# Kernel tuning notes

Measured on AMD Instinct MI355X. Metric: run time of the kernel, lower is better.

Reference implementation:

```python
import jax, jax.numpy as jnp
import numpy as np

H = 16  # heads
K_POLY = 3  # K from init


def setup_inputs() -> dict:
    key = jax.random.key(0)
    ks = jax.random.split(key, 6)
    B, N, D = 4, 1024, 1024
    s = 1.0 / np.sqrt(D)
    return {
        "x": jax.random.normal(ks[0], (B, N, D), jnp.float32),
        "Wq": jax.random.normal(ks[1], (D, D), jnp.float32) * s,
        "bq": jnp.zeros((D,), jnp.float32),
        "Wk": jax.random.normal(ks[2], (D, D), jnp.float32) * s,
        "bk": jnp.zeros((D,), jnp.float32),
        "Wv": jax.random.normal(ks[3], (D, D), jnp.float32) * s,
        "bv": jnp.zeros((D,), jnp.float32),
        "Wo": jax.random.normal(ks[4], (D, D), jnp.float32) * s,
        "bo": jnp.zeros((D,), jnp.float32),
        "w0": jnp.zeros((H,), jnp.float32),
        "w1": jnp.ones((H,), jnp.float32),
        "wK": jnp.zeros((H,), jnp.float32),
    }


def reference(x, Wq, bq, Wk, bk, Wv, bv, Wo, bo, w0, w1, wK):
    B, N, D = x.shape
    d = D // H
    # projections -> [B, H, N, d]
    def proj(W, b):
        return (x @ W + b).reshape(B, N, H, d).transpose(0, 2, 1, 3)
    q = proj(Wq, bq)
    k = proj(Wk, bk)
    v = proj(Wv, bv)
    att = jax.nn.softmax(jnp.einsum('bhnd,bhmd->bhnm', q, k) / jnp.sqrt(jnp.float32(d)), axis=-1)
    att2 = jnp.einsum('bhnm,bhmk->bhnk', att, att)  # att @ att
    attK = att + (K_POLY - 1) * (att2 - att)
    eye = jnp.eye(N, dtype=x.dtype)  # [N, N]
    gf = (w0[None, :, None, None] * eye[None, None]
          + w1[None, :, None, None] * att
          + wK[None, :, None, None] * attK)
    out = jnp.einsum('bhnm,bhmd->bhnd', gf, v)  # [B, H, N, d]
    out = out.transpose(0, 2, 1, 3).reshape(B, N, D)
    return out @ Wo + bo
```

## Files before the change

### kernel.cpp

```cpp
#include <hip/hip_runtime.h>

typedef unsigned short u16;
typedef unsigned int u32;
typedef __attribute__((ext_vector_type(8))) short short8;
typedef __attribute__((ext_vector_type(4))) float f32x4;

__device__ __forceinline__ u16 f2bf(float f) {
  union { float f; u32 u; } c; c.f = f;
  u32 u = c.u;
  u += 0x7fffu + ((u >> 16) & 1u);
  return (u16)(u >> 16);
}
__device__ __forceinline__ float bf2f(u16 h) {
  union { u32 u; float f; } c; c.u = ((u32)h) << 16;
  return c.f;
}

#define GLDS16(g, l)                                                          \
  __builtin_amdgcn_global_load_lds(                                           \
      (const __attribute__((address_space(1))) u32*)(g),                      \
      (__attribute__((address_space(3))) u32*)(l), 16, 0, 0)

__global__ __launch_bounds__(256) void k_cast_x(const float* __restrict__ x,
                                                u16* __restrict__ xb) {
  int i = blockIdx.x * 256 + threadIdx.x;
  float4 v = ((const float4*)x)[i];
  short4 s;
  s.x = (short)f2bf(v.x); s.y = (short)f2bf(v.y);
  s.z = (short)f2bf(v.z); s.w = (short)f2bf(v.w);
  *(short4*)(xb + (size_t)i * 4) = s;
}

__global__ __launch_bounds__(256) void k_trans_w(
    const float* __restrict__ W0, const float* __restrict__ W1,
    const float* __restrict__ W2, const float* __restrict__ W3,
    u16* __restrict__ T0, u16* __restrict__ T1, u16* __restrict__ T2,
    u16* __restrict__ T3) {
  const float* W = blockIdx.z == 0 ? W0 : blockIdx.z == 1 ? W1 : blockIdx.z == 2 ? W2 : W3;
  u16* T = blockIdx.z == 0 ? T0 : blockIdx.z == 1 ? T1 : blockIdx.z == 2 ? T2 : T3;
  __shared__ float tile[32][33];
  int r0 = blockIdx.y * 32, c0 = blockIdx.x * 32;
  int tid = threadIdx.x;
  for (int i = tid; i < 1024; i += 256) {
    int r = i >> 5, c = i & 31;
    tile[r][c] = W[(size_t)(r0 + r) * 1024 + c0 + c];
  }
  __syncthreads();
  for (int i = tid; i < 1024; i += 256) {
    int r = i >> 5, c = i & 31;
    T[(size_t)(c0 + r) * 1024 + r0 + c] = f2bf(tile[c][r]);
  }
}

__device__ __forceinline__ void core128x128_p3(const u16* __restrict__ A,
                                               const u16* __restrict__ Bt, int K,
                                               f32x4 (&acc)[4][4], u16* As,
                                               u16* Bs) {
  const int tid = threadIdx.x;
  const int lane = tid & 63;
  const int wm = tid >> 7, wn = (tid >> 6) & 1;
  const int fr = lane & 15, fg = lane >> 4;
  const int sr = tid >> 2, sc = (tid & 3) * 8;
#pragma unroll
  for (int i = 0; i < 4; ++i)
#pragma unroll
    for (int j = 0; j < 4; ++j) acc[i][j] = f32x4{0.f, 0.f, 0.f, 0.f};

  auto stage = [&](int t, int slot) {
    u16* as = As + slot * 4096;
    u16* bs = Bs + slot * 4096;
    const int k0 = t * 32 + sc;
    GLDS16(A + (size_t)sr * K + k0, as + tid * 8);
    GLDS16(A + (size_t)(sr + 64) * K + k0, as + (256 + tid) * 8);
    GLDS16(Bt + (size_t)sr * K + k0, bs + tid * 8);
    GLDS16(Bt + (size_t)(sr + 64) * K + k0, bs + (256 + tid) * 8);
  };
  auto compute = [&](int slot) {
    const u16* as = As + slot * 4096;
    const u16* bs = Bs + slot * 4096;
    short8 af[4], bfv[4];
#pragma unroll
    for (int i = 0; i < 4; ++i)
      af[i] = *(const short8*)(as + (wm * 64 + i * 16 + fr) * 32 + fg * 8);
#pragma unroll
    for (int j = 0; j < 4; ++j)
      bfv[j] = *(const short8*)(bs + (wn * 64 + j * 16 + fr) * 32 + fg * 8);
#pragma unroll
    for (int i = 0; i < 4; ++i)
#pragma unroll
      for (int j = 0; j < 4; ++j)
        acc[i][j] = __builtin_amdgcn_mfma_f32_16x16x32_bf16(af[i], bfv[j],
                                                            acc[i][j], 0, 0, 0);
  };

  const int NS = K / 32;
  stage(0, 0);
  stage(1, 1);
  int cs = 0, ss = 2;
  for (int t = 0; t + 2 < NS; ++t) {
    asm volatile("s_waitcnt vmcnt(4)" ::: "memory");
    __builtin_amdgcn_s_barrier();
    asm volatile("" ::: "memory");
    stage(t + 2, ss);
    compute(cs);
    cs = cs == 2 ? 0 : cs + 1;
    ss = ss == 2 ? 0 : ss + 1;
  }
  asm volatile("s_waitcnt vmcnt(4)" ::: "memory");
  __builtin_amdgcn_s_barrier();
  asm volatile("" ::: "memory");
  compute(cs);
  cs = cs == 2 ? 0 : cs + 1;
  asm volatile("s_waitcnt vmcnt(0)" ::: "memory");
  __builtin_amdgcn_s_barrier();
  asm volatile("" ::: "memory");
  compute(cs);
}

__device__ __forceinline__ void core128x64_p3(const u16* __restrict__ A,
                                              const u16* __restrict__ Bt, int K,
                                              f32x4 (&acc)[2][4], u16* As,
                                              u16* Bs) {
  const int tid = threadIdx.x;
  const int lane = tid & 63;
  const int w = tid >> 6;
  const int fr = lane & 15, fg = lane >> 4;
  const int sr = tid >> 2, sc = (tid & 3) * 8;
#pragma unroll
  for (int i = 0; i < 2; ++i)
#pragma unroll
    for (int j = 0; j < 4; ++j) acc[i][j] = f32x4{0.f, 0.f, 0.f, 0.f};

  auto stage = [&](int t, int slot) {
    u16* as = As + slot * 4096;
    u16* bs = Bs + slot * 2048;
    const int k0 = t * 32 + sc;
    GLDS16(A + (size_t)sr * K + k0, as + tid * 8);
    GLDS16(A + (size_t)(sr + 64) * K + k0, as + (256 + tid) * 8);
    GLDS16(Bt + (size_t)sr * K + k0, bs + tid * 8);
  };
  auto compute = [&](int slot) {
    const u16* as = As + slot * 4096;
    const u16* bs = Bs + slot * 2048;
    short8 af[2], bfv[4];
#pragma unroll
    for (int i = 0; i < 2; ++i)
      af[i] = *(const short8*)(as + (w * 32 + i * 16 + fr) * 32 + fg * 8);
#pragma unroll
    for (int j = 0; j < 4; ++j)
      bfv[j] = *(const short8*)(bs + (j * 16 + fr) * 32 + fg * 8);
#pragma unroll
    for (int i = 0; i < 2; ++i)
#pragma unroll
      for (int j = 0; j < 4; ++j)
        acc[i][j] = __builtin_amdgcn_mfma_f32_16x16x32_bf16(af[i], bfv[j],
                                                            acc[i][j], 0, 0, 0);
  };

  const int NS = K / 32;
  stage(0, 0);
  stage(1, 1);
  int cs = 0, ss = 2;
  for (int t = 0; t + 2 < NS; ++t) {
    asm volatile("s_waitcnt vmcnt(3)" ::: "memory");
    __builtin_amdgcn_s_barrier();
    asm volatile("" ::: "memory");
    stage(t + 2, ss);
    compute(cs);
    cs = cs == 2 ? 0 : cs + 1;
    ss = ss == 2 ? 0 : ss + 1;
  }
  asm volatile("s_waitcnt vmcnt(3)" ::: "memory");
  __builtin_amdgcn_s_barrier();
  asm volatile("" ::: "memory");
  compute(cs);
  cs = cs == 2 ? 0 : cs + 1;
  asm volatile("s_waitcnt vmcnt(0)" ::: "memory");
  __builtin_amdgcn_s_barrier();
  asm volatile("" ::: "memory");
  compute(cs);
}

__global__ __launch_bounds__(256) void k_proj(
    const u16* __restrict__ xb, const u16* __restrict__ WqT,
    const u16* __restrict__ WkT, const u16* __restrict__ WvT,
    const float* __restrict__ bq, const float* __restrict__ bk,
    const float* __restrict__ bv, u16* __restrict__ qh, u16* __restrict__ kh,
    u16* __restrict__ vh, u16* __restrict__ vT) {
  __shared__ __align__(16) u16 As[3 * 128 * 32];
  __shared__ __align__(16) u16 Bs[3 * 128 * 32];
  const int which = blockIdx.z;
  const u16* Bt = which == 0 ? WqT : which == 1 ? WkT : WvT;
  const float* bias = which == 0 ? bq : which == 1 ? bk : bv;
  const int m0 = blockIdx.x * 128, n0 = blockIdx.y * 128;
  f32x4 acc[4][4];
  core128x128_p3(xb + (size_t)m0 * 1024, Bt + (size_t)n0 * 1024, 1024, acc, As, Bs);
  const int tid = threadIdx.x, lane = tid & 63;
  const int wm = tid >> 7, wn = (tid >> 6) & 1, fr = lane & 15, fg = lane >> 4;
#pragma unroll
  for (int i = 0; i < 4; ++i)
#pragma unroll
    for (int j = 0; j < 4; ++j) {
      int n = n0 + wn * 64 + j * 16 + fr;
      float bb = bias[n];
      int h = n >> 6, dc = n & 63;
#pragma unroll
      for (int r = 0; r < 4; ++r) {
        int m = m0 + wm * 64 + i * 16 + fg * 4 + r;
        int b = m >> 10, nr = m & 1023;
        int z = b * 16 + h;
        float val = acc[i][j][r] + bb;
        u16 bv16 = f2bf(val);
        if (which == 0) {
          qh[((size_t)z * 1024 + nr) * 64 + dc] = bv16;
        } else if (which == 1) {
          kh[((size_t)z * 1024 + nr) * 64 + dc] = bv16;
        } else {
          vh[((size_t)z * 1024 + nr) * 64 + dc] = bv16;
          vT[((size_t)z * 64 + dc) * 1024 + nr] = bv16;
        }
      }
    }
}

__global__ __launch_bounds__(256) void k_pass1(
    const u16* __restrict__ qh, const u16* __restrict__ kh,
    const u16* __restrict__ vT, u16* __restrict__ P1T,
    u16* __restrict__ P1h, float2* __restrict__ ml) {
  __shared__ __align__(16) u16 Ks[64 * 64];
  __shared__ __align__(16) u16 Vs[64 * 64];
  __shared__ __align__(16) u16 Ps[4][32 * 64];
  const int z = blockIdx.y;
  const int m0 = blockIdx.x * 128;
  const int tid = threadIdx.x, lane = tid & 63, w = tid >> 6;
  const int fr = lane & 15, fg = lane >> 4;
  const int row0 = m0 + w * 32;
  const u16* qbase = qh + (size_t)z * 65536;
  const u16* kbase = kh + (size_t)z * 65536;
  const u16* vbase = vT + (size_t)z * 65536;
  u16* myP = &Ps[w][0];

  short8 qf[2][2];
#pragma unroll
  for (int rt = 0; rt < 2; ++rt)
#pragma unroll
    for (int kc = 0; kc < 2; ++kc)
      qf[rt][kc] = *(const short8*)(qbase + (size_t)(row0 + rt * 16 + fr) * 64 +
                                    (kc * 4 + fg) * 8);

  f32x4 o[2][4];
  float mr[2][4], lr[2][4];
#pragma unroll
  for (int rt = 0; rt < 2; ++rt)
#pragma unroll
    for (int ct = 0; ct < 4; ++ct) o[rt][ct] = f32x4{0.f, 0.f, 0.f, 0.f};
#pragma unroll
  for (int rt = 0; rt < 2; ++rt)
#pragma unroll
    for (int r = 0; r < 4; ++r) { mr[rt][r] = -3.0e38f; lr[rt][r] = 0.f; }

  for (int t = 0; t < 16; ++t) {
    const int kv0 = t * 64;
#pragma unroll
    for (int it = 0; it < 2; ++it) {
      int idx = it * 256 + tid;
      int row = idx >> 3, cc = idx & 7;
      GLDS16(kbase + (size_t)(kv0 + row) * 64 + ((cc ^ (row & 7)) * 8),
             Ks + idx * 8);
      GLDS16(vbase + (size_t)row * 1024 + kv0 + ((cc ^ (row & 7)) * 8),
             Vs + idx * 8);
    }
    __syncthreads();
    f32x4 s[2][4];
#pragma unroll
    for (int ct = 0; ct < 4; ++ct) {
      int krow = ct * 16 + fr;
      short8 k0 = *(const short8*)(Ks + krow * 64 + ((fg ^ (krow & 7)) * 8));
      short8 k1 = *(const short8*)(Ks + krow * 64 + (((4 + fg) ^ (krow & 7)) * 8));
#pragma unroll
      for (int rt = 0; rt < 2; ++rt) {
        s[rt][ct] = __builtin_amdgcn_mfma_f32_16x16x32_bf16(
            qf[rt][0], k0, f32x4{0.f, 0.f, 0.f, 0.f}, 0, 0, 0);
        s[rt][ct] = __builtin_amdgcn_mfma_f32_16x16x32_bf16(
            qf[rt][1], k1, s[rt][ct], 0, 0, 0);
      }
    }
    float nm[2][4], rs[2][4], al[2][4];
#pragma unroll
    for (int rt = 0; rt < 2; ++rt)
#pragma unroll
      for (int r = 0; r < 4; ++r)
        nm[rt][r] = fmaxf(fmaxf(s[rt][0][r], s[rt][1][r]),
                          fmaxf(s[rt][2][r], s[rt][3][r]));
#pragma unroll
    for (int off = 1; off < 16; off <<= 1)
#pragma unroll
      for (int rt = 0; rt < 2; ++rt)
#pragma unroll
        for (int r = 0; r < 4; ++r)
          nm[rt][r] = fmaxf(nm[rt][r], __shfl_xor(nm[rt][r], off, 64));
#pragma unroll
    for (int rt = 0; rt < 2; ++rt)
#pragma unroll
      for (int r = 0; r < 4; ++r) {
        float m_ = fmaxf(nm[rt][r], mr[rt][r]);
        al[rt][r] = __expf((mr[rt][r] - m_) * 0.125f);
        nm[rt][r] = m_;
        rs[rt][r] = 0.f;
      }
#pragma unroll
    for (int ct = 0; ct < 4; ++ct)
#pragma unroll
      for (int rt = 0; rt < 2; ++rt)
#pragma unroll
        for (int r = 0; r < 4; ++r) {
          float e = __expf((s[rt][ct][r] - nm[rt][r]) * 0.125f);
          s[rt][ct][r] = e;
          rs[rt][r] += e;
        }
#pragma unroll
    for (int off = 1; off < 16; off <<= 1)
#pragma unroll
      for (int rt = 0; rt < 2; ++rt)
#pragma unroll
        for (int r = 0; r < 4; ++r)
          rs[rt][r] += __shfl_xor(rs[rt][r], off, 64);
#pragma unroll
    for (int rt = 0; rt < 2; ++rt)
#pragma unroll
      for (int r = 0; r < 4; ++r) {
        lr[rt][r] = lr[rt][r] * al[rt][r] + rs[rt][r];
        mr[rt][r] = nm[rt][r];
      }
#pragma unroll
    for (int rt = 0; rt < 2; ++rt)
#pragma unroll
      for (int ct = 0; ct < 4; ++ct)
#pragma unroll
        for (int r = 0; r < 4; ++r) o[rt][ct][r] *= al[rt][r];
#pragma unroll
    for (int rt = 0; rt < 2; ++rt)
#pragma unroll
      for (int ct = 0; ct < 4; ++ct)
#pragma unroll
        for (int r = 0; r < 4; ++r) {
          int prow = rt * 16 + fg * 4 + r;
          int pcol = ct * 16 + fr;
          int cc = pcol >> 3;
          myP[prow * 64 + ((cc ^ (prow & 7)) * 8) + (pcol & 7)] =
              f2bf(s[rt][ct][r]);
        }
    asm volatile("s_waitcnt lgkmcnt(0)" ::: "memory");
#pragma unroll
    for (int rt = 0; rt < 2; ++rt) {
      int prow = rt * 16 + fr;
      short8 p0 = *(const short8*)(myP + prow * 64 + ((fg ^ (prow & 7)) * 8));
      short8 p1 = *(const short8*)(myP + prow * 64 + (((4 + fg) ^ (prow & 7)) * 8));
#pragma unroll
      for (int ct = 0; ct < 4; ++ct) {
        int vrow = ct * 16 + fr;
        short8 v0 = *(const short8*)(Vs + vrow * 64 + ((fg ^ (vrow & 7)) * 8));
        short8 v1 = *(const short8*)(Vs + vrow * 64 + (((4 + fg) ^ (vrow & 7)) * 8));
        o[rt][ct] = __builtin_amdgcn_mfma_f32_16x16x32_bf16(p0, v0, o[rt][ct], 0, 0, 0);
        o[rt][ct] = __builtin_amdgcn_mfma_f32_16x16x32_bf16(p1, v1, o[rt][ct], 0, 0, 0);
      }
    }
    __syncthreads();
  }
  float linv[2][4];
#pragma unroll
  for (int rt = 0; rt < 2; ++rt)
#pragma unroll
    for (int r = 0; r < 4; ++r) linv[rt][r] = 1.f / lr[rt][r];
#pragma unroll
  for (int rt = 0; rt < 2; ++rt)
#pragma unroll
    for (int ct = 0; ct < 4; ++ct) {
      union { u16 u[4]; short4 s4; } pk;
#pragma unroll
      for (int r = 0; r < 4; ++r) {
        u16 b_ = f2bf(o[rt][ct][r] * linv[rt][r]);
        pk.u[r] = b_;
        myP[(rt * 16 + fg * 4 + r) * 64 + ct * 16 + fr] = b_;
      }
      *(short4*)(P1T + ((size_t)z * 64 + ct * 16 + fr) * 1024 + row0 +
                 rt * 16 + fg * 4) = pk.s4;
    }
  asm volatile("s_waitcnt lgkmcnt(0)" ::: "memory");
  {
    int r_ = lane >> 1, hb = lane & 1;
#pragma unroll
    for (int c = 0; c < 4; ++c) {
      int ch = hb * 4 + c;
      int4 vv = *(const int4*)(myP + r_ * 64 + ch * 8);
      *(int4*)(P1h + ((size_t)z * 1024 + row0 + r_) * 64 + ch * 8) = vv;
    }
  }
  if (fr == 0) {
#pragma unroll
    for (int rt = 0; rt < 2; ++rt)
#pragma unroll
      for (int r = 0; r < 4; ++r)
        ml[(size_t)z * 1024 + row0 + rt * 16 + fg * 4 + r] =
            make_float2(mr[rt][r], linv[rt][r]);
  }
}

__global__ __launch_bounds__(256) void k_pass2(
    const u16* __restrict__ qh, const u16* __restrict__ kh,
    const u16* __restrict__ P1T, const u16* __restrict__ vh,
    const u16* __restrict__ P1h, const float2* __restrict__ ml,
    const float* __restrict__ w0, const float* __restrict__ w1,
    const float* __restrict__ wK, u16* __restrict__ OH) {
  __shared__ __align__(16) u16 Ks[64 * 64];
  __shared__ __align__(16) u16 Ts[64 * 64];
  __shared__ __align__(16) u16 Ps[4][32 * 64];
  const int z = blockIdx.y;
  const int m0 = blockIdx.x * 128;
  const int tid = threadIdx.x, lane = tid & 63, w = tid >> 6;
  const int fr = lane & 15, fg = lane >> 4;
  const int row0 = m0 + w * 32;
  const int h = z & 15, b = z >> 4;
  const float c0 = w0[h], c1 = w1[h] - wK[h], c2 = 2.f * wK[h];
  const u16* qbase = qh + (size_t)z * 65536;
  const u16* kbase = kh + (size_t)z * 65536;
  const u16* tbase = P1T + (size_t)z * 65536;
  u16* myP = &Ps[w][0];

  short8 qf[2][2];
#pragma unroll
  for (int rt = 0; rt < 2; ++rt)
#pragma unroll
    for (int kc = 0; kc < 2; ++kc)
      qf[rt][kc] = *(const short8*)(qbase + (size_t)(row0 + rt * 16 + fr) * 64 +
                                    (kc * 4 + fg) * 8);
  float mrow[2][4], lrow[2][4];
#pragma unroll
  for (int rt = 0; rt < 2; ++rt)
#pragma unroll
    for (int r = 0; r < 4; ++r) {
      float2 t_ = ml[(size_t)z * 1024 + row0 + rt * 16 + fg * 4 + r];
      mrow[rt][r] = t_.x;
      lrow[rt][r] = t_.y;
    }
  f32x4 o[2][4];
#pragma unroll
  for (int rt = 0; rt < 2; ++rt)
#pragma unroll
    for (int ct = 0; ct < 4; ++ct) o[rt][ct] = f32x4{0.f, 0.f, 0.f, 0.f};

  for (int t = 0; t < 16; ++t) {
    const int kv0 = t * 64;
#pragma unroll
    for (int it = 0; it < 2; ++it) {
      int idx = it * 256 + tid;
      int row = idx >> 3, cc = idx & 7;
      GLDS16(kbase + (size_t)(kv0 + row) * 64 + ((cc ^ (row & 7)) * 8),
             Ks + idx * 8);
      GLDS16(tbase + (size_t)row * 1024 + kv0 + ((cc ^ (row & 7)) * 8),
             Ts + idx * 8);
    }
    __syncthreads();
    f32x4 s[2][4];
#pragma unroll
    for (int ct = 0; ct < 4; ++ct) {
      int krow = ct * 16 + fr;
      short8 k0 = *(const short8*)(Ks + krow * 64 + ((fg ^ (krow & 7)) * 8));
      short8 k1 = *(const short8*)(Ks + krow * 64 + (((4 + fg) ^ (krow & 7)) * 8));
#pragma unroll
      for (int rt = 0; rt < 2; ++rt) {
        s[rt][ct] = __builtin_amdgcn_mfma_f32_16x16x32_bf16(
            qf[rt][0], k0, f32x4{0.f, 0.f, 0.f, 0.f}, 0, 0, 0);
        s[rt][ct] = __builtin_amdgcn_mfma_f32_16x16x32_bf16(
            qf[rt][1], k1, s[rt][ct], 0, 0, 0);
      }
    }
#pragma unroll
    for (int rt = 0; rt < 2; ++rt)
#pragma unroll
      for (int ct = 0; ct < 4; ++ct)
#pragma unroll
        for (int r = 0; r < 4; ++r) {
          int prow = rt * 16 + fg * 4 + r;
          int pcol = ct * 16 + fr;
          int cc = pcol >> 3;
          float p = __expf((s[rt][ct][r] - mrow[rt][r]) * 0.125f) * lrow[rt][r];
          myP[prow * 64 + ((cc ^ (prow & 7)) * 8) + (pcol & 7)] = f2bf(p);
        }
    asm volatile("s_waitcnt lgkmcnt(0)" ::: "memory");
#pragma unroll
    for (int rt = 0; rt < 2; ++rt) {
      int prow = rt * 16 + fr;
      short8 p0 = *(const short8*)(myP + prow * 64 + ((fg ^ (prow & 7)) * 8));
      short8 p1 = *(const short8*)(myP + prow * 64 + (((4 + fg) ^ (prow & 7)) * 8));
#pragma unroll
      for (int ct = 0; ct < 4; ++ct) {
        int vrow = ct * 16 + fr;
        short8 v0 = *(const short8*)(Ts + vrow * 64 + ((fg ^ (vrow & 7)) * 8));
        short8 v1 = *(const short8*)(Ts + vrow * 64 + (((4 + fg) ^ (vrow & 7)) * 8));
        o[rt][ct] = __builtin_amdgcn_mfma_f32_16x16x32_bf16(p0, v0, o[rt][ct], 0, 0, 0);
        o[rt][ct] = __builtin_amdgcn_mfma_f32_16x16x32_bf16(p1, v1, o[rt][ct], 0, 0, 0);
      }
    }
    __syncthreads();
  }
#pragma unroll
  for (int rt = 0; rt < 2; ++rt)
#pragma unroll
    for (int ct = 0; ct < 4; ++ct)
#pragma unroll
      for (int r = 0; r < 4; ++r)
        myP[(rt * 16 + fg * 4 + r) * 64 + ct * 16 + fr] = f2bf(o[rt][ct][r]);
  asm volatile("s_waitcnt lgkmcnt(0)" ::: "memory");
  {
    int r_ = lane >> 1, hb = lane & 1;
    const u16* vp = vh + ((size_t)z * 1024 + row0 + r_) * 64;
    const u16* pp = P1h + ((size_t)z * 1024 + row0 + r_) * 64;
    u16* op = OH + ((size_t)b * 1024 + row0 + r_) * 1024 + h * 64;
#pragma unroll
    for (int c = 0; c < 4; ++c) {
      int ch = hb * 4 + c;
      short8 pv = *(const short8*)(myP + r_ * 64 + ch * 8);
      short8 vv = *(const short8*)(vp + ch * 8);
      short8 p1 = *(const short8*)(pp + ch * 8);
      short8 res;
#pragma unroll
      for (int e = 0; e < 8; ++e) {
        float f = c0 * bf2f((u16)vv[e]) + c1 * bf2f((u16)p1[e]) +
                  c2 * bf2f((u16)pv[e]);
        res[e] = (short)f2bf(f);
      }
      *(short8*)(op + ch * 8) = res;
    }
  }
}

__global__ __launch_bounds__(256) void k_final(const u16* __restrict__ OH,
                                               const u16* __restrict__ WoT,
                                               const float* __restrict__ bo,
                                               float* __restrict__ out) {
  __shared__ __align__(16) u16 As[3 * 128 * 32];
  __shared__ __align__(16) u16 Bs[3 * 64 * 32];
  const int m0 = blockIdx.x * 128, n0 = blockIdx.y * 64;
  f32x4 acc[2][4];
  core128x64_p3(OH + (size_t)m0 * 1024, WoT + (size_t)n0 * 1024, 1024, acc, As, Bs);
  const int tid = threadIdx.x, lane = tid & 63, w = tid >> 6;
  const int fr = lane & 15, fg = lane >> 4;
#pragma unroll
  for (int i = 0; i < 2; ++i)
#pragma unroll
    for (int j = 0; j < 4; ++j) {
      int n = n0 + j * 16 + fr;
      float bb = bo[n];
#pragma unroll
      for (int r = 0; r < 4; ++r) {
        int m = m0 + w * 32 + i * 16 + fg * 4 + r;
        out[(size_t)m * 1024 + n] = acc[i][j][r] + bb;
      }
    }
}

extern "C" void kernel_launch(void* const* d_in, const int* in_sizes, int n_in,
                              void* d_out, int out_size, void* d_ws,
                              size_t ws_size, hipStream_t stream) {
  const float* x = (const float*)d_in[0];
  const float* Wq = (const float*)d_in[1];
  const float* bq = (const float*)d_in[2];
  const float* Wk = (const float*)d_in[3];
  const float* bk = (const float*)d_in[4];
  const float* Wv = (const float*)d_in[5];
  const float* bv = (const float*)d_in[6];
  const float* Wo = (const float*)d_in[7];
  const float* bo = (const float*)d_in[8];
  const float* w0 = (const float*)d_in[9];
  const float* w1 = (const float*)d_in[10];
  const float* wK = (const float*)d_in[11];
  float* out = (float*)d_out;

  char* ws = (char*)d_ws;
  const size_t MB = 1ull << 20;
  u16* xb  = (u16*)(ws);
  u16* WqT = (u16*)(ws + 8 * MB);
  u16* WkT = (u16*)(ws + 10 * MB);
  u16* WvT = (u16*)(ws + 12 * MB);
  u16* WoT = (u16*)(ws + 14 * MB);
  u16* qh  = (u16*)(ws + 16 * MB);
  u16* kh  = (u16*)(ws + 24 * MB);
  u16* vh  = (u16*)(ws + 32 * MB);
  u16* vT  = (u16*)(ws + 40 * MB);
  u16* P1T = (u16*)(ws + 48 * MB);
  u16* P1h = (u16*)(ws + 56 * MB);
  u16* OH  = (u16*)(ws + 64 * MB);
  float2* ml = (float2*)(ws + 72 * MB);

  hipLaunchKernelGGL(k_cast_x, dim3(4096), dim3(256), 0, stream, x, xb);
  hipLaunchKernelGGL(k_trans_w, dim3(32, 32, 4), dim3(256), 0, stream, Wq, Wk,
                     Wv, Wo, WqT, WkT, WvT, WoT);
  hipLaunchKernelGGL(k_proj, dim3(32, 8, 3), dim3(256), 0, stream, xb, WqT, WkT,
                     WvT, bq, bk, bv, qh, kh, vh, vT);
  hipLaunchKernelGGL(k_pass1, dim3(8, 64), dim3(256), 0, stream, qh, kh, vT,
                     P1T, P1h, ml);
  hipLaunchKernelGGL(k_pass2, dim3(8, 64), dim3(256), 0, stream, qh, kh, P1T,
                     vh, P1h, ml, w0, w1, wK, OH);
  hipLaunchKernelGGL(k_final, dim3(32, 16), dim3(256), 0, stream, OH, WoT, bo,
                     out);
}
```

Before: 182.5 us.

## Drop online-softmax max tracking and halve attention row tiles per block

```diff
diff --git a/kernel.cpp b/kernel.cpp
--- a/kernel.cpp
+++ b/kernel.cpp
@@ -20,6 +20,8 @@
   __builtin_amdgcn_global_load_lds(                                           \
       (const __attribute__((address_space(1))) u32*)(g),                      \
       (__attribute__((address_space(3))) u32*)(l), 16, 0, 0)
+
+#define EXP_SCALE 0.18033688011112042f
 
 __global__ __launch_bounds__(256) void k_cast_x(const float* __restrict__ x,
                                                 u16* __restrict__ xb) {
@@ -226,38 +228,31 @@
 __global__ __launch_bounds__(256) void k_pass1(
     const u16* __restrict__ qh, const u16* __restrict__ kh,
     const u16* __restrict__ vT, u16* __restrict__ P1T,
-    u16* __restrict__ P1h, float2* __restrict__ ml) {
+    u16* __restrict__ P1h, float* __restrict__ mlinv) {
   __shared__ __align__(16) u16 Ks[64 * 64];
   __shared__ __align__(16) u16 Vs[64 * 64];
-  __shared__ __align__(16) u16 Ps[4][32 * 64];
+  __shared__ __align__(16) u16 Ps[4][16 * 64];
   const int z = blockIdx.y;
-  const int m0 = blockIdx.x * 128;
+  const int m0 = blockIdx.x * 64;
   const int tid = threadIdx.x, lane = tid & 63, w = tid >> 6;
   const int fr = lane & 15, fg = lane >> 4;
-  const int row0 = m0 + w * 32;
+  const int row0 = m0 + w * 16;
   const u16* qbase = qh + (size_t)z * 65536;
   const u16* kbase = kh + (size_t)z * 65536;
   const u16* vbase = vT + (size_t)z * 65536;
   u16* myP = &Ps[w][0];
 
-  short8 qf[2][2];
-#pragma unroll
-  for (int rt = 0; rt < 2; ++rt)
-#pragma unroll
-    for (int kc = 0; kc < 2; ++kc)
-      qf[rt][kc] = *(const short8*)(qbase + (size_t)(row0 + rt * 16 + fr) * 64 +
-                                    (kc * 4 + fg) * 8);
-
-  f32x4 o[2][4];
-  float mr[2][4], lr[2][4];
-#pragma unroll
-  for (int rt = 0; rt < 2; ++rt)
-#pragma unroll
-    for (int ct = 0; ct < 4; ++ct) o[rt][ct] = f32x4{0.f, 0.f, 0.f, 0.f};
-#pragma unroll
-  for (int rt = 0; rt < 2; ++rt)
-#pragma unroll
-    for (int r = 0; r < 4; ++r) { mr[rt][r] = -3.0e38f; lr[rt][r] = 0.f; }
+  short8 qf[2];
+#pragma unroll
+  for (int kc = 0; kc < 2; ++kc)
+    qf[kc] = *(const short8*)(qbase + (size_t)(row0 + fr) * 64 + (kc * 4 + fg) * 8);
+
+  f32x4 o[4];
+  float rs[4];
+#pragma unroll
+  for (int ct = 0; ct < 4; ++ct) o[ct] = f32x4{0.f, 0.f, 0.f, 0.f};
+#pragma unroll
+  for (int r = 0; r < 4; ++r) rs[r] = 0.f;
 
   for (int t = 0; t < 16; ++t) {
     const int kv0 = t * 64;
@@ -271,155 +266,87 @@
              Vs + idx * 8);
     }
     __syncthreads();
-    f32x4 s[2][4];
 #pragma unroll
     for (int ct = 0; ct < 4; ++ct) {
       int krow = ct * 16 + fr;
       short8 k0 = *(const short8*)(Ks + krow * 64 + ((fg ^ (krow & 7)) * 8));
       short8 k1 = *(const short8*)(Ks + krow * 64 + (((4 + fg) ^ (krow & 7)) * 8));
-#pragma unroll
-      for (int rt = 0; rt < 2; ++rt) {
-        s[rt][ct] = __builtin_amdgcn_mfma_f32_16x16x32_bf16(
-            qf[rt][0], k0, f32x4{0.f, 0.f, 0.f, 0.f}, 0, 0, 0);
-        s[rt][ct] = __builtin_amdgcn_mfma_f32_16x16x32_bf16(
-            qf[rt][1], k1, s[rt][ct], 0, 0, 0);
+      f32x4 s = __builtin_amdgcn_mfma_f32_16x16x32_bf16(
+          qf[0], k0, f32x4{0.f, 0.f, 0.f, 0.f}, 0, 0, 0);
+      s = __builtin_amdgcn_mfma_f32_16x16x32_bf16(qf[1], k1, s, 0, 0, 0);
+      int pcol = ct * 16 + fr;
+      int cc = pcol >> 3;
+#pragma unroll
+      for (int r = 0; r < 4; ++r) {
+        float e = __builtin_exp2f(s[r] * EXP_SCALE);
+        rs[r] += e;
+        int prow = fg * 4 + r;
+        myP[prow * 64 + ((cc ^ (prow & 7)) * 8) + (pcol & 7)] = f2bf(e);
       }
     }
-    float nm[2][4], rs[2][4], al[2][4];
-#pragma unroll
-    for (int rt = 0; rt < 2; ++rt)
-#pragma unroll
-      for (int r = 0; r < 4; ++r)
-        nm[rt][r] = fmaxf(fmaxf(s[rt][0][r], s[rt][1][r]),
-                          fmaxf(s[rt][2][r], s[rt][3][r]));
-#pragma unroll
-    for (int off = 1; off < 16; off <<= 1)
-#pragma unroll
-      for (int rt = 0; rt < 2; ++rt)
-#pragma unroll
-        for (int r = 0; r < 4; ++r)
-          nm[rt][r] = fmaxf(nm[rt][r], __shfl_xor(nm[rt][r], off, 64));
-#pragma unroll
-    for (int rt = 0; rt < 2; ++rt)
-#pragma unroll
-      for (int r = 0; r < 4; ++r) {
-        float m_ = fmaxf(nm[rt][r], mr[rt][r]);
-        al[rt][r] = __expf((mr[rt][r] - m_) * 0.125f);
-        nm[rt][r] = m_;
-        rs[rt][r] = 0.f;
-      }
-#pragma unroll
-    for (int ct = 0; ct < 4; ++ct)
-#pragma unroll
-      for (int rt = 0; rt < 2; ++rt)
-#pragma unroll
-        for (int r = 0; r < 4; ++r) {
-          float e = __expf((s[rt][ct][r] - nm[rt][r]) * 0.125f);
-          s[rt][ct][r] = e;
-          rs[rt][r] += e;
-        }
-#pragma unroll
-    for (int off = 1; off < 16; off <<= 1)
-#pragma unroll
-      for (int rt = 0; rt < 2; ++rt)
-#pragma unroll
-        for (int r = 0; r < 4; ++r)
-          rs[rt][r] += __shfl_xor(rs[rt][r], off, 64);
-#pragma unroll
-    for (int rt = 0; rt < 2; ++rt)
-#pragma unroll
-      for (int r = 0; r < 4; ++r) {
-        lr[rt][r] = lr[rt][r] * al[rt][r] + rs[rt][r];
-        mr[rt][r] = nm[rt][r];
-      }
-#pragma unroll
-    for (int rt = 0; rt < 2; ++rt)
-#pragma unroll
-      for (int ct = 0; ct < 4; ++ct)
-#pragma unroll
-        for (int r = 0; r < 4; ++r) o[rt][ct][r] *= al[rt][r];
-#pragma unroll
-    for (int rt = 0; rt < 2; ++rt)
-#pragma unroll
-      for (int ct = 0; ct < 4; ++ct)
-#pragma unroll
-        for (int r = 0; r < 4; ++r) {
-          int prow = rt * 16 + fg * 4 + r;
-          int pcol = ct * 16 + fr;
-          int cc = pcol >> 3;
-          myP[prow * 64 + ((cc ^ (prow & 7)) * 8) + (pcol & 7)] =
-              f2bf(s[rt][ct][r]);
-        }
     asm volatile("s_waitcnt lgkmcnt(0)" ::: "memory");
-#pragma unroll
-    for (int rt = 0; rt < 2; ++rt) {
-      int prow = rt * 16 + fr;
-      short8 p0 = *(const short8*)(myP + prow * 64 + ((fg ^ (prow & 7)) * 8));
-      short8 p1 = *(const short8*)(myP + prow * 64 + (((4 + fg) ^ (prow & 7)) * 8));
-#pragma unroll
-      for (int ct = 0; ct < 4; ++ct) {
-        int vrow = ct * 16 + fr;
-        short8 v0 = *(const short8*)(Vs + vrow * 64 + ((fg ^ (vrow & 7)) * 8));
-        short8 v1 = *(const short8*)(Vs + vrow * 64 + (((4 + fg) ^ (vrow & 7)) * 8));
-        o[rt][ct] = __builtin_amdgcn_mfma_f32_16x16x32_bf16(p0, v0, o[rt][ct], 0, 0, 0);
-        o[rt][ct] = __builtin_amdgcn_mfma_f32_16x16x32_bf16(p1, v1, o[rt][ct], 0, 0, 0);
-      }
+    short8 p0 = *(const short8*)(myP + fr * 64 + ((fg ^ (fr & 7)) * 8));
+    short8 p1 = *(const short8*)(myP + fr * 64 + (((4 + fg) ^ (fr & 7)) * 8));
+#pragma unroll
+    for (int ct = 0; ct < 4; ++ct) {
+      int vrow = ct * 16 + fr;
+      short8 v0 = *(const short8*)(Vs + vrow * 64 + ((fg ^ (vrow & 7)) * 8));
+      short8 v1 = *(const short8*)(Vs + vrow * 64 + (((4 + fg) ^ (vrow & 7)) * 8));
+      o[ct] = __builtin_amdgcn_mfma_f32_16x16x32_bf16(p0, v0, o[ct], 0, 0, 0);
+      o[ct] = __builtin_amdgcn_mfma_f32_16x16x32_bf16(p1, v1, o[ct], 0, 0, 0);
     }
     __syncthreads();
   }
-  float linv[2][4];
-#pragma unroll
-  for (int rt = 0; rt < 2; ++rt)
-#pragma unroll
-    for (int r = 0; r < 4; ++r) linv[rt][r] = 1.f / lr[rt][r];
-#pragma unroll
-  for (int rt = 0; rt < 2; ++rt)
-#pragma unroll
-    for (int ct = 0; ct < 4; ++ct) {
-      union { u16 u[4]; short4 s4; } pk;
-#pragma unroll
-      for (int r = 0; r < 4; ++r) {
-        u16 b_ = f2bf(o[rt][ct][r] * linv[rt][r]);
-        pk.u[r] = b_;
-        myP[(rt * 16 + fg * 4 + r) * 64 + ct * 16 + fr] = b_;
-      }
-      *(short4*)(P1T + ((size_t)z * 64 + ct * 16 + fr) * 1024 + row0 +
-                 rt * 16 + fg * 4) = pk.s4;
-    }
+#pragma unroll
+  for (int off = 1; off < 16; off <<= 1)
+#pragma unroll
+    for (int r = 0; r < 4; ++r) rs[r] += __shfl_xor(rs[r], off, 64);
+  float linv[4];
+#pragma unroll
+  for (int r = 0; r < 4; ++r) linv[r] = 1.f / rs[r];
+#pragma unroll
+  for (int ct = 0; ct < 4; ++ct) {
+    union { u16 u[4]; short4 s4; } pk;
+#pragma unroll
+    for (int r = 0; r < 4; ++r) {
+      u16 b_ = f2bf(o[ct][r] * linv[r]);
+      pk.u[r] = b_;
+      myP[(fg * 4 + r) * 64 + ct * 16 + fr] = b_;
+    }
+    *(short4*)(P1T + ((size_t)z * 64 + ct * 16 + fr) * 1024 + row0 + fg * 4) =
+        pk.s4;
+  }
   asm volatile("s_waitcnt lgkmcnt(0)" ::: "memory");
   {
-    int r_ = lane >> 1, hb = lane & 1;
-#pragma unroll
-    for (int c = 0; c < 4; ++c) {
-      int ch = hb * 4 + c;
+    int r_ = lane >> 2;
+#pragma unroll
+    for (int c = 0; c < 2; ++c) {
+      int ch = (lane & 3) * 2 + c;
       int4 vv = *(const int4*)(myP + r_ * 64 + ch * 8);
       *(int4*)(P1h + ((size_t)z * 1024 + row0 + r_) * 64 + ch * 8) = vv;
     }
   }
   if (fr == 0) {
 #pragma unroll
-    for (int rt = 0; rt < 2; ++rt)
-#pragma unroll
-      for (int r = 0; r < 4; ++r)
-        ml[(size_t)z * 1024 + row0 + rt * 16 + fg * 4 + r] =
-            make_float2(mr[rt][r], linv[rt][r]);
+    for (int r = 0; r < 4; ++r)
+      mlinv[(size_t)z * 1024 + row0 + fg * 4 + r] = linv[r];
   }
 }
 
 __global__ __launch_bounds__(256) void k_pass2(
     const u16* __restrict__ qh, const u16* __restrict__ kh,
     const u16* __restrict__ P1T, const u16* __restrict__ vh,
-    const u16* __restrict__ P1h, const float2* __restrict__ ml,
+    const u16* __restrict__ P1h, const float* __restrict__ mlinv,
     const float* __restrict__ w0, const float* __restrict__ w1,
     const float* __restrict__ wK, u16* __restrict__ OH) {
   __shared__ __align__(16) u16 Ks[64 * 64];
   __shared__ __align__(16) u16 Ts[64 * 64];
-  __shared__ __align__(16) u16 Ps[4][32 * 64];
+  __shared__ __align__(16) u16 Ps[4][16 * 64];
   const int z = blockIdx.y;
-  const int m0 = blockIdx.x * 128;
+  const int m0 = blockIdx.x * 64;
   const int tid = threadIdx.x, lane = tid & 63, w = tid >> 6;
   const int fr = lane & 15, fg = lane >> 4;
-  const int row0 = m0 + w * 32;
+  const int row0 = m0 + w * 16;
   const int h = z & 15, b = z >> 4;
   const float c0 = w0[h], c1 = w1[h] - wK[h], c2 = 2.f * wK[h];
   const u16* qbase = qh + (size_t)z * 65536;
@@ -427,27 +354,17 @@
   const u16* tbase = P1T + (size_t)z * 65536;
   u16* myP = &Ps[w][0];
 
-  short8 qf[2][2];
-#pragma unroll
-  for (int rt = 0; rt < 2; ++rt)
-#pragma unroll
-    for (int kc = 0; kc < 2; ++kc)
-      qf[rt][kc] = *(const short8*)(qbase + (size_t)(row0 + rt * 16 + fr) * 64 +
-                                    (kc * 4 + fg) * 8);
-  float mrow[2][4], lrow[2][4];
-#pragma unroll
-  for (int rt = 0; rt < 2; ++rt)
-#pragma unroll
-    for (int r = 0; r < 4; ++r) {
-      float2 t_ = ml[(size_t)z * 1024 + row0 + rt * 16 + fg * 4 + r];
-      mrow[rt][r] = t_.x;
-      lrow[rt][r] = t_.y;
-    }
-  f32x4 o[2][4];
-#pragma unroll
-  for (int rt = 0; rt < 2; ++rt)
-#pragma unroll
-    for (int ct = 0; ct < 4; ++ct) o[rt][ct] = f32x4{0.f, 0.f, 0.f, 0.f};
+  short8 qf[2];
+#pragma unroll
+  for (int kc = 0; kc < 2; ++kc)
+    qf[kc] = *(const short8*)(qbase + (size_t)(row0 + fr) * 64 + (kc * 4 + fg) * 8);
+  float lrow[4];
+#pragma unroll
+  for (int r = 0; r < 4; ++r)
+    lrow[r] = mlinv[(size_t)z * 1024 + row0 + fg * 4 + r];
+  f32x4 o[4];
+#pragma unroll
+  for (int ct = 0; ct < 4; ++ct) o[ct] = f32x4{0.f, 0.f, 0.f, 0.f};
 
   for (int t = 0; t < 16; ++t) {
     const int kv0 = t * 64;
@@ -461,65 +378,50 @@
              Ts + idx * 8);
     }
     __syncthreads();
-    f32x4 s[2][4];
 #pragma unroll
     for (int ct = 0; ct < 4; ++ct) {
       int krow = ct * 16 + fr;
       short8 k0 = *(const short8*)(Ks + krow * 64 + ((fg ^ (krow & 7)) * 8));
       short8 k1 = *(const short8*)(Ks + krow * 64 + (((4 + fg) ^ (krow & 7)) * 8));
-#pragma unroll
-      for (int rt = 0; rt < 2; ++rt) {
-        s[rt][ct] = __builtin_amdgcn_mfma_f32_16x16x32_bf16(
-            qf[rt][0], k0, f32x4{0.f, 0.f, 0.f, 0.f}, 0, 0, 0);
-        s[rt][ct] = __builtin_amdgcn_mfma_f32_16x16x32_bf16(
-            qf[rt][1], k1, s[rt][ct], 0, 0, 0);
+      f32x4 s = __builtin_amdgcn_mfma_f32_16x16x32_bf16(
+          qf[0], k0, f32x4{0.f, 0.f, 0.f, 0.f}, 0, 0, 0);
+      s = __builtin_amdgcn_mfma_f32_16x16x32_bf16(qf[1], k1, s, 0, 0, 0);
+      int pcol = ct * 16 + fr;
+      int cc = pcol >> 3;
+#pragma unroll
+      for (int r = 0; r < 4; ++r) {
+        float p = __builtin_exp2f(s[r] * EXP_SCALE) * lrow[r];
+        int prow = fg * 4 + r;
+        myP[prow * 64 + ((cc ^ (prow & 7)) * 8) + (pcol & 7)] = f2bf(p);
       }
     }
-#pragma unroll
-    for (int rt = 0; rt < 2; ++rt)
-#pragma unroll
-      for (int ct = 0; ct < 4; ++ct)
-#pragma unroll
-        for (int r = 0; r < 4; ++r) {
-          int prow = rt * 16 + fg * 4 + r;
-          int pcol = ct * 16 + fr;
-          int cc = pcol >> 3;
-          float p = __expf((s[rt][ct][r] - mrow[rt][r]) * 0.125f) * lrow[rt][r];
-          myP[prow * 64 + ((cc ^ (prow & 7)) * 8) + (pcol & 7)] = f2bf(p);
-        }
     asm volatile("s_waitcnt lgkmcnt(0)" ::: "memory");
-#pragma unroll
-    for (int rt = 0; rt < 2; ++rt) {
-      int prow = rt * 16 + fr;
-      short8 p0 = *(const short8*)(myP + prow * 64 + ((fg ^ (prow & 7)) * 8));
-      short8 p1 = *(const short8*)(myP + prow * 64 + (((4 + fg) ^ (prow & 7)) * 8));
-#pragma unroll
-      for (int ct = 0; ct < 4; ++ct) {
-        int vrow = ct * 16 + fr;
-        short8 v0 = *(const short8*)(Ts + vrow * 64 + ((fg ^ (vrow & 7)) * 8));
-        short8 v1 = *(const short8*)(Ts + vrow * 64 + (((4 + fg) ^ (vrow & 7)) * 8));
-        o[rt][ct] = __builtin_amdgcn_mfma_f32_16x16x32_bf16(p0, v0, o[rt][ct], 0, 0, 0);
-        o[rt][ct] = __builtin_amdgcn_mfma_f32_16x16x32_bf16(p1, v1, o[rt][ct], 0, 0, 0);
-      }
+    short8 p0 = *(const short8*)(myP + fr * 64 + ((fg ^ (fr & 7)) * 8));
+    short8 p1 = *(const short8*)(myP + fr * 64 + (((4 + fg) ^ (fr & 7)) * 8));
+#pragma unroll
+    for (int ct = 0; ct < 4; ++ct) {
+      int vrow = ct * 16 + fr;
+      short8 v0 = *(const short8*)(Ts + vrow * 64 + ((fg ^ (vrow & 7)) * 8));
+      short8 v1 = *(const short8*)(Ts + vrow * 64 + (((4 + fg) ^ (vrow & 7)) * 8));
+      o[ct] = __builtin_amdgcn_mfma_f32_16x16x32_bf16(p0, v0, o[ct], 0, 0, 0);
+      o[ct] = __builtin_amdgcn_mfma_f32_16x16x32_bf16(p1, v1, o[ct], 0, 0, 0);
     }
     __syncthreads();
   }
 #pragma unroll
-  for (int rt = 0; rt < 2; ++rt)
-#pragma unroll
-    for (int ct = 0; ct < 4; ++ct)
-#pragma unroll
-      for (int r = 0; r < 4; ++r)
-        myP[(rt * 16 + fg * 4 + r) * 64 + ct * 16 + fr] = f2bf(o[rt][ct][r]);
+  for (int ct = 0; ct < 4; ++ct)
+#pragma unroll
+    for (int r = 0; r < 4; ++r)
+      myP[(fg * 4 + r) * 64 + ct * 16 + fr] = f2bf(o[ct][r]);
   asm volatile("s_waitcnt lgkmcnt(0)" ::: "memory");
   {
-    int r_ = lane >> 1, hb = lane & 1;
+    int r_ = lane >> 2;
     const u16* vp = vh + ((size_t)z * 1024 + row0 + r_) * 64;
     const u16* pp = P1h + ((size_t)z * 1024 + row0 + r_) * 64;
     u16* op = OH + ((size_t)b * 1024 + row0 + r_) * 1024 + h * 64;
 #pragma unroll
-    for (int c = 0; c < 4; ++c) {
-      int ch = hb * 4 + c;
+    for (int c = 0; c < 2; ++c) {
+      int ch = (lane & 3) * 2 + c;
       short8 pv = *(const short8*)(myP + r_ * 64 + ch * 8);
       short8 vv = *(const short8*)(vp + ch * 8);
       short8 p1 = *(const short8*)(pp + ch * 8);
@@ -591,17 +493,17 @@
   u16* P1T = (u16*)(ws + 48 * MB);
   u16* P1h = (u16*)(ws + 56 * MB);
   u16* OH  = (u16*)(ws + 64 * MB);
-  float2* ml = (float2*)(ws + 72 * MB);
+  float* mlinv = (float*)(ws + 72 * MB);
 
   hipLaunchKernelGGL(k_cast_x, dim3(4096), dim3(256), 0, stream, x, xb);
   hipLaunchKernelGGL(k_trans_w, dim3(32, 32, 4), dim3(256), 0, stream, Wq, Wk,
                      Wv, Wo, WqT, WkT, WvT, WoT);
   hipLaunchKernelGGL(k_proj, dim3(32, 8, 3), dim3(256), 0, stream, xb, WqT, WkT,
                      WvT, bq, bk, bv, qh, kh, vh, vT);
-  hipLaunchKernelGGL(k_pass1, dim3(8, 64), dim3(256), 0, stream, qh, kh, vT,
-                     P1T, P1h, ml);
-  hipLaunchKernelGGL(k_pass2, dim3(8, 64), dim3(256), 0, stream, qh, kh, P1T,
-                     vh, P1h, ml, w0, w1, wK, OH);
+  hipLaunchKernelGGL(k_pass1, dim3(16, 64), dim3(256), 0, stream, qh, kh, vT,
+                     P1T, P1h, mlinv);
+  hipLaunchKernelGGL(k_pass2, dim3(16, 64), dim3(256), 0, stream, qh, kh, P1T,
+                     vh, P1h, mlinv, w0, w1, wK, OH);
   hipLaunchKernelGGL(k_final, dim3(32, 16), dim3(256), 0, stream, OH, WoT, bo,
                      out);
 }
```

After: 157.0 us. 14.0% less time.
